# Kernel tuning notes

Hardware: AMD Instinct MI355X
Metric: run time of the kernel (lower is better)

Reference implementation:

```python
import jax, jax.numpy as jnp
import numpy as np

B, S, D = 4, 128, 4096
H, KV, HD = 32, 8, 128
REP = H // KV  # GQA repeat factor = 4


def setup_inputs() -> dict:
    key = jax.random.key(0)
    ks = jax.random.split(key, 10)
    scale = 0.02
    x = jax.random.normal(ks[0], (B, S, D), dtype=jnp.float32)
    # projection weights stored as (in, out) so y = x @ W + b (== torch Linear)
    wq = jax.random.normal(ks[1], (D, H * HD), dtype=jnp.float32) * scale
    bq = jax.random.normal(ks[2], (H * HD,), dtype=jnp.float32) * scale
    wk = jax.random.normal(ks[3], (D, KV * HD), dtype=jnp.float32) * scale
    bk = jax.random.normal(ks[4], (KV * HD,), dtype=jnp.float32) * scale
    wv = jax.random.normal(ks[5], (D, KV * HD), dtype=jnp.float32) * scale
    bv = jax.random.normal(ks[6], (KV * HD,), dtype=jnp.float32) * scale
    wo = jax.random.normal(ks[7], (H * HD, D), dtype=jnp.float32) * scale
    bo = jax.random.normal(ks[8], (D,), dtype=jnp.float32) * scale
    # rotary frequencies: theta=10000, half-dim = HD//2 = 64
    inv_freq = 1.0 / (10000.0 ** (jnp.arange(0, HD, 2, dtype=jnp.float32) / HD))
    t = jnp.arange(S, dtype=jnp.float32)
    angles = jnp.outer(t, inv_freq)  # (S, 64)
    freqs_cos = jnp.cos(angles)
    freqs_sin = jnp.sin(angles)
    # additive causal mask (S, S): 0 on/below diagonal, -inf above
    mask = jnp.where(jnp.tril(jnp.ones((S, S), dtype=bool)), 0.0, -jnp.inf).astype(jnp.float32)
    cache_k = jnp.zeros((B, S, KV, HD), dtype=jnp.float32)
    cache_v = jnp.zeros((B, S, KV, HD), dtype=jnp.float32)
    return {
        "x": x, "start_pos": 0, "freqs_cos": freqs_cos, "freqs_sin": freqs_sin,
        "mask": mask, "cache_k": cache_k, "cache_v": cache_v,
        "wq": wq, "bq": bq, "wk": wk, "bk": bk, "wv": wv, "bv": bv,
        "wo": wo, "bo": bo,
    }


def _rope(t, cos, sin):
    # t: (B, S, h, HD); treat last dim as HD//2 complex pairs (real, imag)
    tr = t.reshape(*t.shape[:-1], HD // 2, 2)
    tre, tim = tr[..., 0], tr[..., 1]
    c = cos[None, :, None, :]  # (1, S, 1, HD//2)
    s = sin[None, :, None, :]
    out_re = tre * c - tim * s
    out_im = tre * s + tim * c
    return jnp.stack([out_re, out_im], axis=-1).reshape(t.shape)


def reference(x, start_pos, freqs_cos, freqs_sin, mask, cache_k, cache_v,
              wq, bq, wk, bk, wv, bv, wo, bo):
    bsz, seq_len, _ = x.shape
    q = (x @ wq + bq).reshape(bsz, seq_len, H, HD)
    k = (x @ wk + bk).reshape(bsz, seq_len, KV, HD)
    v = (x @ wv + bv).reshape(bsz, seq_len, KV, HD)
    q = _rope(q, freqs_cos, freqs_sin)
    k = _rope(k, freqs_cos, freqs_sin)
    # KV-cache append (functional)
    cache_k = cache_k.at[:bsz, start_pos:start_pos + seq_len].set(k)
    cache_v = cache_v.at[:bsz, start_pos:start_pos + seq_len].set(v)
    keys = cache_k[:bsz, :start_pos + seq_len]    # (B, T, KV, HD)
    vals = cache_v[:bsz, :start_pos + seq_len]
    # GQA head expansion (repeat_interleave on head dim)
    keys = jnp.repeat(keys, REP, axis=2)          # (B, T, H, HD)
    vals = jnp.repeat(vals, REP, axis=2)
    scale = 1.0 / jnp.sqrt(jnp.float32(HD))
    scores = jnp.einsum('bqhd,bkhd->bhqk', q, keys) * scale + mask
    attn = jax.nn.softmax(scores, axis=-1)
    out = jnp.einsum('bhqk,bkhd->bqhd', attn, vals).reshape(bsz, seq_len, H * HD)
    return out @ wo + bo
```

## Files before the change

kernel.cpp:

```cpp
#include <hip/hip_runtime.h>
#include <math.h>


#define B_   4
#define S_   128
#define D_   4096
#define H_   32
#define KV_  8
#define HD_  128
#define M_   (B_ * S_)
#define NQKV 6144
#define SCALE_ 0.088388347648318447f

typedef _Float16 half_t;
typedef half_t f16x8 __attribute__((ext_vector_type(8)));
typedef float  f32x4 __attribute__((ext_vector_type(4)));

__device__ inline void load_lds16(const void* g, void* l) {
    __builtin_amdgcn_global_load_lds((const __attribute__((address_space(1))) void*)g,
                                     (__attribute__((address_space(3))) void*)l,
                                     16, 0, 0);
}

__device__ void transpose_tile(const float* __restrict__ src, int Nsrc, int nsrc0,
                               int ndst0, int k0, int Ntot,
                               half_t* __restrict__ Wt, void* ldsraw) {
    float (*tile)[132] = (float(*)[132])ldsraw;
    const int t = threadIdx.x;
#pragma unroll
    for (int p = 0; p < 8; ++p) {
        int idx = t + p * 256;
        int r = idx >> 5, c4 = idx & 31;
        *(float4*)&tile[r][c4 * 4] =
            *(const float4*)&src[(size_t)(k0 + r) * Nsrc + nsrc0 + c4 * 4];
    }
    __syncthreads();
    const int n = t >> 1, kh = t & 1;
    __align__(16) half_t hs[32];
#pragma unroll
    for (int i = 0; i < 32; ++i)
        hs[i] = (half_t)tile[kh * 32 + i][n];
    size_t ob = ((size_t)(k0 >> 6) * Ntot + ndst0 + n) * 64 + kh * 32;
#pragma unroll
    for (int u = 0; u < 4; ++u)
        *(uint4*)&Wt[ob + u * 8] = *(uint4*)&hs[u * 8];
}

__global__ __launch_bounds__(256)
void prep_qkv(const float* __restrict__ wq, const float* __restrict__ wk,
              const float* __restrict__ wv, const float* __restrict__ x,
              half_t* __restrict__ Wt, half_t* __restrict__ x16) {
    __shared__ __align__(16) char lds[33792];
    const int bx = blockIdx.x;
    if (bx < 3072) {
        int nt = bx % 48, kt = bx / 48;
        const float* src; int Nsrc, ns0, nd0;
        if (nt < 32)      { src = wq; Nsrc = 4096; ns0 = nt * 128;        nd0 = nt * 128; }
        else if (nt < 40) { src = wk; Nsrc = 1024; ns0 = (nt - 32) * 128; nd0 = 4096 + (nt - 32) * 128; }
        else              { src = wv; Nsrc = 1024; ns0 = (nt - 40) * 128; nd0 = 5120 + (nt - 40) * 128; }
        transpose_tile(src, Nsrc, ns0, nd0, kt * 64, NQKV, Wt, lds);
    } else {
        int i0 = (bx - 3072) * 1024 + threadIdx.x;
#pragma unroll
        for (int j = 0; j < 4; ++j) {
            int i = i0 + j * 256;
            float4 f = ((const float4*)x)[i];
            __align__(8) half_t h4[4] = {(half_t)f.x, (half_t)f.y, (half_t)f.z, (half_t)f.w};
            ((uint2*)x16)[i] = *(uint2*)h4;
        }
    }
}

__device__ __forceinline__ void stage64x128(const half_t* __restrict__ A,
                                            const half_t* __restrict__ Bbase,
                                            int N, int m0, int n0, int kc,
                                            half_t* AsD, half_t* BsD, int tid) {
    const int lane = tid & 63, tB = tid & 192;
    const half_t* Bslab = Bbase + ((size_t)(kc >> 6) * N + n0) * 64;
#pragma unroll
    for (int p = 0; p < 2; ++p) {
        int tb = p * 256 + tB;
        int task = tb + lane;
        int r = task >> 3, os = (task ^ r) & 7;
        load_lds16(&A[(size_t)(m0 + r) * 4096 + kc + os * 8], AsD + tb * 8);
    }
#pragma unroll
    for (int p = 0; p < 4; ++p) {
        int tb = p * 256 + tB;
        int task = tb + lane;
        int r = task >> 3, os = (task ^ r) & 7;
        load_lds16(&Bslab[(size_t)r * 64 + os * 8], BsD + tb * 8);
    }
}

__device__ __forceinline__ void compute64x128(const half_t* AsD, const half_t* BsD,
                                              int tid, f32x4 (&acc)[4][2]) {
    const int lane = tid & 63;
    const int quad = lane >> 4, l16 = lane & 15;
    const int wn = (tid >> 6) * 32;
    half_t (*As)[64] = (half_t(*)[64])AsD;
    half_t (*Bs)[64] = (half_t(*)[64])BsD;
#pragma unroll
    for (int kk = 0; kk < 2; ++kk) {
        f16x8 af[4], bf[2];
        int L = kk * 4 + quad;
#pragma unroll
        for (int i = 0; i < 4; ++i) {
            int ra = i * 16 + l16;
            af[i] = *(const f16x8*)&As[ra][(L ^ (ra & 7)) * 8];
        }
#pragma unroll
        for (int j = 0; j < 2; ++j) {
            int rb = wn + j * 16 + l16;
            bf[j] = *(const f16x8*)&Bs[rb][(L ^ (rb & 7)) * 8];
        }
#pragma unroll
        for (int i = 0; i < 4; ++i)
#pragma unroll
            for (int j = 0; j < 2; ++j)
                acc[i][j] = __builtin_amdgcn_mfma_f32_16x16x32_f16(af[i], bf[j], acc[i][j], 0, 0, 0);
    }
}

__device__ __forceinline__ void fence_step(int n) {
    if (n == 6)      asm volatile("s_waitcnt vmcnt(6)" ::: "memory");
    else if (n == 0) asm volatile("s_waitcnt vmcnt(0)" ::: "memory");
    __builtin_amdgcn_s_barrier();
    __builtin_amdgcn_sched_barrier(0);
}

__device__ __forceinline__ void gemm64x128(const half_t* __restrict__ A,
                                           const half_t* __restrict__ Bbase,
                                           int N, int m0, int n0, char* lds,
                                           f32x4 (&acc)[4][2]) {
    const int tid = threadIdx.x;
    half_t* As0 = (half_t*)lds;
    half_t* Bs0 = (half_t*)(lds + 24576);
    stage64x128(A, Bbase, N, m0, n0, 0,  As0,        Bs0,        tid);
    stage64x128(A, Bbase, N, m0, n0, 64, As0 + 4096, Bs0 + 8192, tid);
    fence_step(6);
    int cur = 0, pf = 2;
    for (int it = 0; it < 62; ++it) {
        stage64x128(A, Bbase, N, m0, n0, (it + 2) * 64,
                    As0 + pf * 4096, Bs0 + pf * 8192, tid);
        compute64x128(As0 + cur * 4096, Bs0 + cur * 8192, tid, acc);
        fence_step(6);
        cur = (cur == 2) ? 0 : cur + 1;
        pf  = (pf  == 2) ? 0 : pf  + 1;
    }
    compute64x128(As0 + cur * 4096, Bs0 + cur * 8192, tid, acc);
    fence_step(0);
    cur = (cur == 2) ? 0 : cur + 1;
    compute64x128(As0 + cur * 4096, Bs0 + cur * 8192, tid, acc);
    __syncthreads();
}

__global__ __launch_bounds__(256, 2)
void gemm_qkv_fused(const half_t* __restrict__ x16, const half_t* __restrict__ Wt,
                    const float* __restrict__ bq, const float* __restrict__ bk,
                    const float* __restrict__ bv, const float* __restrict__ fc,
                    const float* __restrict__ fs, half_t* __restrict__ q16,
                    half_t* __restrict__ k16, half_t* __restrict__ vt16) {
    __shared__ __align__(16) char lds[73728];
    const int bx = blockIdx.x;
    const int o = (bx & 7) * 48 + (bx >> 3);
    const int nb = o >> 3, mb = o & 7;
    const int m0 = mb * 64, n0 = nb * 128;

    f32x4 acc[4][2] = {};
    gemm64x128(x16, Wt, NQKV, m0, n0, lds, acc);

    const int tid = threadIdx.x;
    const int lane = tid & 63;
    const int quad = lane >> 4, l16 = lane & 15;
    const int wn = (tid >> 6) * 32;

    if (n0 < 5120) {
        const bool isQ = n0 < 4096;
        const float* bias = isQ ? bq : bk;
        const int bOff = isQ ? 0 : 4096;
        half_t* dst = isQ ? q16 : k16;
        const int ldd = isQ ? 4096 : 1024;
#pragma unroll
        for (int i = 0; i < 4; ++i)
#pragma unroll
            for (int j = 0; j < 2; ++j) {
                const int col = n0 + wn + j * 16 + l16;
                const int d2 = (col >> 1) & 63;
                const float bcol = bias[col - bOff];
#pragma unroll
                for (int rg = 0; rg < 4; ++rg) {
                    const int row = m0 + i * 16 + quad * 4 + rg;
                    float v = acc[i][j][rg] + bcol;
                    float p = __shfl_xor(v, 1);
                    const int iloc = row & 127;
                    const float c = fc[iloc * 64 + d2], sn = fs[iloc * 64 + d2];
                    float ov = (l16 & 1) ? (p * sn + v * c)
                                         : (v * c - p * sn);
                    float o2 = __shfl_xor(ov, 1);
                    if (!(l16 & 1)) {
                        __align__(4) half_t hh[2] = {(half_t)ov, (half_t)o2};
                        *(unsigned int*)&dst[(size_t)row * ldd + (col - bOff)] =
                            *(unsigned int*)hh;
                    }
                }
            }
    } else {
        half_t (*Th)[136] = (half_t(*)[136])lds;
#pragma unroll
        for (int i = 0; i < 4; ++i)
#pragma unroll
            for (int j = 0; j < 2; ++j) {
                const int cl = wn + j * 16 + l16;
                const float bcol = bv[n0 - 5120 + cl];
#pragma unroll
                for (int rg = 0; rg < 4; ++rg)
                    Th[i * 16 + quad * 4 + rg][cl] = (half_t)(acc[i][j][rg] + bcol);
            }
        __syncthreads();
        const int d = tid >> 1, ih = tid & 1;
        const int kv = (n0 - 5120) >> 7;
        const int b = mb >> 1, i0 = (mb & 1) * 64;
        __align__(16) half_t hs[32];
#pragma unroll
        for (int u = 0; u < 32; ++u) hs[u] = Th[ih * 32 + u][d];
        size_t base = ((size_t)(b * 8 + kv) * 128 + d) * 128 + i0 + ih * 32;
#pragma unroll
        for (int u = 0; u < 4; ++u)
            *(uint4*)&vt16[base + u * 8] = *(uint4*)&hs[u * 8];
    }
}

__global__ __launch_bounds__(256, 2)
void attn_wo(const half_t* __restrict__ q16, const half_t* __restrict__ k16,
             const half_t* __restrict__ vt16, half_t* __restrict__ a16,
             const float* __restrict__ wo, half_t* __restrict__ WtO) {
    __shared__ __align__(16) char lds[62464];
    if (blockIdx.x >= 512) {
        int t = blockIdx.x - 512;
        transpose_tile(wo, 4096, (t & 31) * 128, (t & 31) * 128, (t >> 5) * 64,
                       4096, WtO, lds);
        return;
    }
    half_t (*Qs)[136] = (half_t(*)[136])lds;
    half_t (*Ks)[136] = (half_t(*)[136])(lds + 8704);
    float (*Ps)[132]  = (float(*)[132])(lds + 43520);
    float (*red)[16]  = (float(*)[16])(lds + 60416);

    const int tid = threadIdx.x;
    const int qi = blockIdx.x & 3, h = (blockIdx.x >> 2) & 31, b = blockIdx.x >> 7;
    const int kv = h >> 2;
    const int qbase = qi * 32;
    const int lane = tid & 63, w = tid >> 6;
    const int quad = lane >> 4, l16 = lane & 15;
    const int m0 = (w & 1) * 16, half64 = (w >> 1) * 64;

#pragma unroll
    for (int p = 0; p < 2; ++p) {
        int task = tid + p * 256;
        int r = task >> 4, c = task & 15;
        *(uint4*)&Qs[r][c * 8] =
            *(const uint4*)&q16[((size_t)(b * 128 + qbase + r) * 32 + h) * 128 + c * 8];
    }
#pragma unroll
    for (int p = 0; p < 8; ++p) {
        int task = tid + p * 256;
        int r = task >> 4, c = task & 15;
        *(uint4*)&Ks[r][c * 8] =
            *(const uint4*)&k16[((size_t)(b * 128 + r) * 8 + kv) * 128 + c * 8];
    }
    __syncthreads();

    f32x4 s[4] = {};
#pragma unroll
    for (int kc = 0; kc < 4; ++kc) {
        f16x8 af = *(const f16x8*)&Qs[m0 + l16][kc * 32 + quad * 8];
#pragma unroll
        for (int jb = 0; jb < 4; ++jb) {
            f16x8 bf = *(const f16x8*)&Ks[half64 + jb * 16 + l16][kc * 32 + quad * 8];
            s[jb] = __builtin_amdgcn_mfma_f32_16x16x32_f16(af, bf, s[jb], 0, 0, 0);
        }
    }
#pragma unroll
    for (int jb = 0; jb < 4; ++jb) {
        int j = half64 + jb * 16 + l16;
#pragma unroll
        for (int rg = 0; rg < 4; ++rg) {
            int row = m0 + quad * 4 + rg;
            Ps[row][j] = (j <= qbase + row) ? s[jb][rg] * SCALE_ : -1e30f;
        }
    }
    __syncthreads();

    const int r = tid >> 3, seg = tid & 7;
    float mx = -1e30f;
#pragma unroll
    for (int i = 0; i < 16; ++i) mx = fmaxf(mx, Ps[r][seg * 16 + i]);
    red[r][seg] = mx;
    __syncthreads();

    uint4 vstage[8];
#pragma unroll
    for (int p = 0; p < 8; ++p) {
        int task = tid + p * 256;
        int rr = task >> 4, c = task & 15;
        vstage[p] = *(const uint4*)&vt16[((size_t)(b * 8 + kv) * 128 + rr) * 128 + c * 8];
    }
    float m = red[r][0];
#pragma unroll
    for (int i = 1; i < 8; ++i) m = fmaxf(m, red[r][i]);
    float sum = 0.f;
#pragma unroll
    for (int i = 0; i < 16; ++i) {
        float e = __expf(Ps[r][seg * 16 + i] - m);
        Ps[r][seg * 16 + i] = e;
        sum += e;
    }
    red[r][8 + seg] = sum;
#pragma unroll
    for (int p = 0; p < 8; ++p) {
        int task = tid + p * 256;
        int rr = task >> 4, c = task & 15;
        *(uint4*)&Ks[rr][c * 8] = vstage[p];
    }
    __syncthreads();

    float tot = 0.f;
#pragma unroll
    for (int i = 0; i < 8; ++i) tot += red[r][8 + i];
    float inv = 1.0f / tot;
#pragma unroll
    for (int i = 0; i < 16; ++i)
        Qs[r][seg * 16 + i] = (half_t)(Ps[r][seg * 16 + i] * inv);
    __syncthreads();

    f32x4 o[4] = {};
#pragma unroll
    for (int jc = 0; jc < 4; ++jc) {
        f16x8 af = *(const f16x8*)&Qs[m0 + l16][jc * 32 + quad * 8];
#pragma unroll
        for (int db = 0; db < 4; ++db) {
            f16x8 bf = *(const f16x8*)&Ks[half64 + db * 16 + l16][jc * 32 + quad * 8];
            o[db] = __builtin_amdgcn_mfma_f32_16x16x32_f16(af, bf, o[db], 0, 0, 0);
        }
    }
#pragma unroll
    for (int db = 0; db < 4; ++db) {
        int d = half64 + db * 16 + l16;
#pragma unroll
        for (int rg = 0; rg < 4; ++rg) {
            int row = m0 + quad * 4 + rg;
            a16[(size_t)(b * 128 + qbase + row) * 4096 + h * 128 + d] = (half_t)o[db][rg];
        }
    }
}

__global__ __launch_bounds__(256, 2)
void gemm_o_fused(const half_t* __restrict__ a16, const half_t* __restrict__ WtO,
                  const float* __restrict__ bo, float* __restrict__ out) {
    __shared__ __align__(16) char lds[73728];
    const int bx = blockIdx.x;
    const int o = (bx & 7) * 32 + (bx >> 3);
    const int nb = o >> 3, mb = o & 7;
    const int m0 = mb * 64, n0 = nb * 128;

    f32x4 acc[4][2] = {};
    gemm64x128(a16, WtO, 4096, m0, n0, lds, acc);

    const int tid = threadIdx.x;
    const int lane = tid & 63;
    const int quad = lane >> 4, l16 = lane & 15;
    const int wn = (tid >> 6) * 32;
#pragma unroll
    for (int i = 0; i < 4; ++i)
#pragma unroll
        for (int j = 0; j < 2; ++j) {
            const int col = n0 + wn + j * 16 + l16;
            const float bcol = bo[col];
#pragma unroll
            for (int rg = 0; rg < 4; ++rg) {
                const int row = m0 + i * 16 + quad * 4 + rg;
                out[(size_t)row * 4096 + col] = acc[i][j][rg] + bcol;
            }
        }
}

extern "C" void kernel_launch(void* const* d_in, const int* in_sizes, int n_in,
                              void* d_out, int out_size, void* d_ws, size_t ws_size,
                              hipStream_t stream) {
    const float* x    = (const float*)d_in[0];
    const float* fc   = (const float*)d_in[2];
    const float* fs   = (const float*)d_in[3];
    const float* wq   = (const float*)d_in[7];
    const float* bq   = (const float*)d_in[8];
    const float* wk   = (const float*)d_in[9];
    const float* bk   = (const float*)d_in[10];
    const float* wv   = (const float*)d_in[11];
    const float* bv   = (const float*)d_in[12];
    const float* wo   = (const float*)d_in[13];
    const float* bo   = (const float*)d_in[14];
    float* out = (float*)d_out;

    half_t* x16  = (half_t*)d_ws;
    half_t* a16  = x16 + 2097152;
    half_t* q16  = a16 + 2097152;
    half_t* k16  = q16 + 2097152;
    half_t* vt16 = k16 + 524288;
    half_t* Wt   = vt16 + 524288;
    half_t* WtO  = Wt;

    prep_qkv<<<3584, 256, 0, stream>>>(wq, wk, wv, x, Wt, x16);

    gemm_qkv_fused<<<384, 256, 0, stream>>>(x16, Wt, bq, bk, bv, fc, fs,
                                            q16, k16, vt16);

    attn_wo<<<2560, 256, 0, stream>>>(q16, k16, vt16, a16, wo, WtO);

    gemm_o_fused<<<256, 256, 0, stream>>>(a16, WtO, bo, out);
}
```

Before: 283.1 us.

## Shrink GEMM tiles to 32x128, move Wo transpose into prep, swizzle transpose LDS

The QKV and output GEMMs move from 64x128 to 32x128 tiles, doubling grid sizes to 768 and 512 blocks for better CU occupancy on small M. The Wo weight transpose moves out of the attention kernel into a single combined prep kernel with its own workspace buffer. The transpose tile gets an XOR-swizzled LDS layout and coalesced 16-byte stores to cut bank conflicts. Smaller tiles reload more B data per unit of work, and the prep kernel now does more work before the QKV GEMM can start.

```diff
diff --git a/kernel.cpp b/kernel.cpp
--- a/kernel.cpp
+++ b/kernel.cpp
@@ -31,25 +31,32 @@
     for (int p = 0; p < 8; ++p) {
         int idx = t + p * 256;
         int r = idx >> 5, c4 = idx & 31;
-        *(float4*)&tile[r][c4 * 4] =
+        *(float4*)&tile[r][((c4 ^ ((r >> 3) & 7)) * 4)] =
             *(const float4*)&src[(size_t)(k0 + r) * Nsrc + nsrc0 + c4 * 4];
     }
     __syncthreads();
-    const int n = t >> 1, kh = t & 1;
-    __align__(16) half_t hs[32];
-#pragma unroll
-    for (int i = 0; i < 32; ++i)
-        hs[i] = (half_t)tile[kh * 32 + i][n];
-    size_t ob = ((size_t)(k0 >> 6) * Ntot + ndst0 + n) * 64 + kh * 32;
-#pragma unroll
-    for (int u = 0; u < 4; ++u)
-        *(uint4*)&Wt[ob + u * 8] = *(uint4*)&hs[u * 8];
+    const int kh = (t >> 2) & 1, cc = t & 3, dd = t >> 3;
+    const int rbase = kh * 32 + cc * 8;
+    const int h3 = 4 * kh + cc;
+    size_t tb = ((size_t)(k0 >> 6) * Ntot + ndst0) * 64;
+#pragma unroll
+    for (int u = 0; u < 4; ++u) {
+        int n = u * 32 + dd;
+        int pc = ((n >> 2) ^ h3) * 4 + (n & 3);
+        __align__(16) half_t hs[8];
+#pragma unroll
+        for (int i = 0; i < 8; ++i)
+            hs[i] = (half_t)tile[rbase + i][pc];
+        *(uint4*)&Wt[tb + (size_t)u * 2048 + t * 8] = *(uint4*)hs;
+    }
 }
 
 __global__ __launch_bounds__(256)
-void prep_qkv(const float* __restrict__ wq, const float* __restrict__ wk,
-              const float* __restrict__ wv, const float* __restrict__ x,
-              half_t* __restrict__ Wt, half_t* __restrict__ x16) {
+void prep_all(const float* __restrict__ wq, const float* __restrict__ wk,
+              const float* __restrict__ wv, const float* __restrict__ wo,
+              const float* __restrict__ x,
+              half_t* __restrict__ Wt, half_t* __restrict__ WtO,
+              half_t* __restrict__ x16) {
     __shared__ __align__(16) char lds[33792];
     const int bx = blockIdx.x;
     if (bx < 3072) {
@@ -59,7 +66,7 @@
         else if (nt < 40) { src = wk; Nsrc = 1024; ns0 = (nt - 32) * 128; nd0 = 4096 + (nt - 32) * 128; }
         else              { src = wv; Nsrc = 1024; ns0 = (nt - 40) * 128; nd0 = 5120 + (nt - 40) * 128; }
         transpose_tile(src, Nsrc, ns0, nd0, kt * 64, NQKV, Wt, lds);
-    } else {
+    } else if (bx < 3584) {
         int i0 = (bx - 3072) * 1024 + threadIdx.x;
 #pragma unroll
         for (int j = 0; j < 4; ++j) {
@@ -68,21 +75,23 @@
             __align__(8) half_t h4[4] = {(half_t)f.x, (half_t)f.y, (half_t)f.z, (half_t)f.w};
             ((uint2*)x16)[i] = *(uint2*)h4;
         }
-    }
-}
-
-__device__ __forceinline__ void stage64x128(const half_t* __restrict__ A,
+    } else {
+        int tw = bx - 3584;
+        transpose_tile(wo, 4096, (tw & 31) * 128, (tw & 31) * 128,
+                       (tw >> 5) * 64, 4096, WtO, lds);
+    }
+}
+
+__device__ __forceinline__ void stage32x128(const half_t* __restrict__ A,
                                             const half_t* __restrict__ Bbase,
                                             int N, int m0, int n0, int kc,
                                             half_t* AsD, half_t* BsD, int tid) {
     const int lane = tid & 63, tB = tid & 192;
     const half_t* Bslab = Bbase + ((size_t)(kc >> 6) * N + n0) * 64;
-#pragma unroll
-    for (int p = 0; p < 2; ++p) {
-        int tb = p * 256 + tB;
-        int task = tb + lane;
+    {
+        int task = tB + lane;
         int r = task >> 3, os = (task ^ r) & 7;
-        load_lds16(&A[(size_t)(m0 + r) * 4096 + kc + os * 8], AsD + tb * 8);
+        load_lds16(&A[(size_t)(m0 + r) * 4096 + kc + os * 8], AsD + tB * 8);
     }
 #pragma unroll
     for (int p = 0; p < 4; ++p) {
@@ -93,8 +102,8 @@
     }
 }
 
-__device__ __forceinline__ void compute64x128(const half_t* AsD, const half_t* BsD,
-                                              int tid, f32x4 (&acc)[4][2]) {
+__device__ __forceinline__ void compute32x128(const half_t* AsD, const half_t* BsD,
+                                              int tid, f32x4 (&acc)[2][2]) {
     const int lane = tid & 63;
     const int quad = lane >> 4, l16 = lane & 15;
     const int wn = (tid >> 6) * 32;
@@ -102,10 +111,10 @@
     half_t (*Bs)[64] = (half_t(*)[64])BsD;
 #pragma unroll
     for (int kk = 0; kk < 2; ++kk) {
-        f16x8 af[4], bf[2];
+        f16x8 af[2], bf[2];
         int L = kk * 4 + quad;
 #pragma unroll
-        for (int i = 0; i < 4; ++i) {
+        for (int i = 0; i < 2; ++i) {
             int ra = i * 16 + l16;
             af[i] = *(const f16x8*)&As[ra][(L ^ (ra & 7)) * 8];
         }
@@ -115,7 +124,7 @@
             bf[j] = *(const f16x8*)&Bs[rb][(L ^ (rb & 7)) * 8];
         }
 #pragma unroll
-        for (int i = 0; i < 4; ++i)
+        for (int i = 0; i < 2; ++i)
 #pragma unroll
             for (int j = 0; j < 2; ++j)
                 acc[i][j] = __builtin_amdgcn_mfma_f32_16x16x32_f16(af[i], bf[j], acc[i][j], 0, 0, 0);
@@ -123,35 +132,35 @@
 }
 
 __device__ __forceinline__ void fence_step(int n) {
-    if (n == 6)      asm volatile("s_waitcnt vmcnt(6)" ::: "memory");
+    if (n == 5)      asm volatile("s_waitcnt vmcnt(5)" ::: "memory");
     else if (n == 0) asm volatile("s_waitcnt vmcnt(0)" ::: "memory");
     __builtin_amdgcn_s_barrier();
     __builtin_amdgcn_sched_barrier(0);
 }
 
-__device__ __forceinline__ void gemm64x128(const half_t* __restrict__ A,
+__device__ __forceinline__ void gemm32x128(const half_t* __restrict__ A,
                                            const half_t* __restrict__ Bbase,
                                            int N, int m0, int n0, char* lds,
-                                           f32x4 (&acc)[4][2]) {
+                                           f32x4 (&acc)[2][2]) {
     const int tid = threadIdx.x;
     half_t* As0 = (half_t*)lds;
-    half_t* Bs0 = (half_t*)(lds + 24576);
-    stage64x128(A, Bbase, N, m0, n0, 0,  As0,        Bs0,        tid);
-    stage64x128(A, Bbase, N, m0, n0, 64, As0 + 4096, Bs0 + 8192, tid);
-    fence_step(6);
+    half_t* Bs0 = (half_t*)(lds + 12288);
+    stage32x128(A, Bbase, N, m0, n0, 0,  As0,        Bs0,        tid);
+    stage32x128(A, Bbase, N, m0, n0, 64, As0 + 2048, Bs0 + 8192, tid);
+    fence_step(5);
     int cur = 0, pf = 2;
     for (int it = 0; it < 62; ++it) {
-        stage64x128(A, Bbase, N, m0, n0, (it + 2) * 64,
-                    As0 + pf * 4096, Bs0 + pf * 8192, tid);
-        compute64x128(As0 + cur * 4096, Bs0 + cur * 8192, tid, acc);
-        fence_step(6);
+        stage32x128(A, Bbase, N, m0, n0, (it + 2) * 64,
+                    As0 + pf * 2048, Bs0 + pf * 8192, tid);
+        compute32x128(As0 + cur * 2048, Bs0 + cur * 8192, tid, acc);
+        fence_step(5);
         cur = (cur == 2) ? 0 : cur + 1;
         pf  = (pf  == 2) ? 0 : pf  + 1;
     }
-    compute64x128(As0 + cur * 4096, Bs0 + cur * 8192, tid, acc);
+    compute32x128(As0 + cur * 2048, Bs0 + cur * 8192, tid, acc);
     fence_step(0);
     cur = (cur == 2) ? 0 : cur + 1;
-    compute64x128(As0 + cur * 4096, Bs0 + cur * 8192, tid, acc);
+    compute32x128(As0 + cur * 2048, Bs0 + cur * 8192, tid, acc);
     __syncthreads();
 }
 
@@ -161,14 +170,14 @@
                     const float* __restrict__ bv, const float* __restrict__ fc,
                     const float* __restrict__ fs, half_t* __restrict__ q16,
                     half_t* __restrict__ k16, half_t* __restrict__ vt16) {
-    __shared__ __align__(16) char lds[73728];
+    __shared__ __align__(16) char lds[61440];
     const int bx = blockIdx.x;
-    const int o = (bx & 7) * 48 + (bx >> 3);
-    const int nb = o >> 3, mb = o & 7;
-    const int m0 = mb * 64, n0 = nb * 128;
-
-    f32x4 acc[4][2] = {};
-    gemm64x128(x16, Wt, NQKV, m0, n0, lds, acc);
+    const int o = (bx & 7) * 96 + (bx >> 3);
+    const int nb = o >> 4, mb = o & 15;
+    const int m0 = mb * 32, n0 = nb * 128;
+
+    f32x4 acc[2][2] = {};
+    gemm32x128(x16, Wt, NQKV, m0, n0, lds, acc);
 
     const int tid = threadIdx.x;
     const int lane = tid & 63;
@@ -182,7 +191,7 @@
         half_t* dst = isQ ? q16 : k16;
         const int ldd = isQ ? 4096 : 1024;
 #pragma unroll
-        for (int i = 0; i < 4; ++i)
+        for (int i = 0; i < 2; ++i)
 #pragma unroll
             for (int j = 0; j < 2; ++j) {
                 const int col = n0 + wn + j * 16 + l16;
@@ -208,7 +217,7 @@
     } else {
         half_t (*Th)[136] = (half_t(*)[136])lds;
 #pragma unroll
-        for (int i = 0; i < 4; ++i)
+        for (int i = 0; i < 2; ++i)
 #pragma unroll
             for (int j = 0; j < 2; ++j) {
                 const int cl = wn + j * 16 + l16;
@@ -220,28 +229,21 @@
         __syncthreads();
         const int d = tid >> 1, ih = tid & 1;
         const int kv = (n0 - 5120) >> 7;
-        const int b = mb >> 1, i0 = (mb & 1) * 64;
-        __align__(16) half_t hs[32];
-#pragma unroll
-        for (int u = 0; u < 32; ++u) hs[u] = Th[ih * 32 + u][d];
-        size_t base = ((size_t)(b * 8 + kv) * 128 + d) * 128 + i0 + ih * 32;
-#pragma unroll
-        for (int u = 0; u < 4; ++u)
+        const int b = mb >> 2, i0 = (mb & 3) * 32;
+        __align__(16) half_t hs[16];
+#pragma unroll
+        for (int u = 0; u < 16; ++u) hs[u] = Th[ih * 16 + u][d];
+        size_t base = ((size_t)(b * 8 + kv) * 128 + d) * 128 + i0 + ih * 16;
+#pragma unroll
+        for (int u = 0; u < 2; ++u)
             *(uint4*)&vt16[base + u * 8] = *(uint4*)&hs[u * 8];
     }
 }
 
 __global__ __launch_bounds__(256, 2)
-void attn_wo(const half_t* __restrict__ q16, const half_t* __restrict__ k16,
-             const half_t* __restrict__ vt16, half_t* __restrict__ a16,
-             const float* __restrict__ wo, half_t* __restrict__ WtO) {
+void fused_attn(const half_t* __restrict__ q16, const half_t* __restrict__ k16,
+                const half_t* __restrict__ vt16, half_t* __restrict__ a16) {
     __shared__ __align__(16) char lds[62464];
-    if (blockIdx.x >= 512) {
-        int t = blockIdx.x - 512;
-        transpose_tile(wo, 4096, (t & 31) * 128, (t & 31) * 128, (t >> 5) * 64,
-                       4096, WtO, lds);
-        return;
-    }
     half_t (*Qs)[136] = (half_t(*)[136])lds;
     half_t (*Ks)[136] = (half_t(*)[136])(lds + 8704);
     float (*Ps)[132]  = (float(*)[132])(lds + 43520);
@@ -358,21 +360,21 @@
 __global__ __launch_bounds__(256, 2)
 void gemm_o_fused(const half_t* __restrict__ a16, const half_t* __restrict__ WtO,
                   const float* __restrict__ bo, float* __restrict__ out) {
-    __shared__ __align__(16) char lds[73728];
+    __shared__ __align__(16) char lds[61440];
     const int bx = blockIdx.x;
-    const int o = (bx & 7) * 32 + (bx >> 3);
-    const int nb = o >> 3, mb = o & 7;
-    const int m0 = mb * 64, n0 = nb * 128;
-
-    f32x4 acc[4][2] = {};
-    gemm64x128(a16, WtO, 4096, m0, n0, lds, acc);
+    const int o = (bx & 7) * 64 + (bx >> 3);
+    const int nb = o >> 4, mb = o & 15;
+    const int m0 = mb * 32, n0 = nb * 128;
+
+    f32x4 acc[2][2] = {};
+    gemm32x128(a16, WtO, 4096, m0, n0, lds, acc);
 
     const int tid = threadIdx.x;
     const int lane = tid & 63;
     const int quad = lane >> 4, l16 = lane & 15;
     const int wn = (tid >> 6) * 32;
 #pragma unroll
-    for (int i = 0; i < 4; ++i)
+    for (int i = 0; i < 2; ++i)
 #pragma unroll
         for (int j = 0; j < 2; ++j) {
             const int col = n0 + wn + j * 16 + l16;
@@ -407,14 +409,14 @@
     half_t* k16  = q16 + 2097152;
     half_t* vt16 = k16 + 524288;
     half_t* Wt   = vt16 + 524288;
-    half_t* WtO  = Wt;
-
-    prep_qkv<<<3584, 256, 0, stream>>>(wq, wk, wv, x, Wt, x16);
-
-    gemm_qkv_fused<<<384, 256, 0, stream>>>(x16, Wt, bq, bk, bv, fc, fs,
+    half_t* WtO  = Wt + 25165824;
+
+    prep_all<<<5632, 256, 0, stream>>>(wq, wk, wv, wo, x, Wt, WtO, x16);
+
+    gemm_qkv_fused<<<768, 256, 0, stream>>>(x16, Wt, bq, bk, bv, fc, fs,
                                             q16, k16, vt16);
 
-    attn_wo<<<2560, 256, 0, stream>>>(q16, k16, vt16, a16, wo, WtO);
-
-    gemm_o_fused<<<256, 256, 0, stream>>>(a16, WtO, bo, out);
-}
+    fused_attn<<<512, 256, 0, stream>>>(q16, k16, vt16, a16);
+
+    gemm_o_fused<<<512, 256, 0, stream>>>(a16, WtO, bo, out);
+}
```

Measured after the change: 298.3 us. 5.4% more time.
